# Kernel tuning notes

Measured on AMD Instinct MI355X. Metric: run time of the kernel, lower is better.

The kernel has to match this reference:

```python
import jax, jax.numpy as jnp
import numpy as np

POI, EMB, UNITS, QDIM, B = 5000, 256, 512, 256, 64


def setup_inputs() -> dict:
    key = jax.random.key(0)
    ks = jax.random.split(key, 16)
    s = 0.05
    return {
        "x": jax.random.randint(ks[0], (B,), 0, POI),
        "query": jax.random.normal(ks[1], (B, QDIM), jnp.float32),
        "poi_embedding": jax.random.normal(ks[2], (POI, EMB), jnp.float32),
        "A_hat": jax.random.normal(ks[3], (B, B), jnp.float32),
        "dec_hidden": jax.random.normal(ks[4], (B, UNITS), jnp.float32),
        "cat_dec_hidden": jax.random.normal(ks[5], (1, B, UNITS), jnp.float32),
        # GRUCell params (keras order z, r, h; reset_after=True -> bias [2, 3*units])
        "gru_kernel": jax.random.normal(ks[6], (EMB + QDIM, 3 * UNITS), jnp.float32) * s,
        "gru_rec_kernel": jax.random.normal(ks[7], (UNITS, 3 * UNITS), jnp.float32) * s,
        "gru_bias": jax.random.normal(ks[8], (2, 3 * UNITS), jnp.float32) * s,
        # Bahdanau attention params
        "W1_w": jax.random.normal(ks[9], (EMB, UNITS), jnp.float32) * s,
        "W1_b": jnp.zeros((UNITS,), jnp.float32),
        "W2_w": jax.random.normal(ks[10], (UNITS, UNITS), jnp.float32) * s,
        "W2_b": jnp.zeros((UNITS,), jnp.float32),
        "V_w": jax.random.normal(ks[11], (UNITS, 1), jnp.float32) * s,
        "V_b": jnp.zeros((1,), jnp.float32),
        # output dense: concat(context EMB, output_ UNITS, cat_hidden UNITS) -> POI
        "fc_w": jax.random.normal(ks[12], (EMB + 2 * UNITS, POI), jnp.float32) * s,
        "fc_b": jnp.zeros((POI,), jnp.float32),
    }


def _gru_cell(x, h, kernel, rec_kernel, bias):
    # keras GRUCell, reset_after=True, gate order (z, r, h)
    xm = x @ kernel + bias[0]        # [B, 3U]
    hm = h @ rec_kernel + bias[1]    # [B, 3U]
    xz, xr, xh = jnp.split(xm, 3, axis=-1)
    hz, hr, hh = jnp.split(hm, 3, axis=-1)
    z = jax.nn.sigmoid(xz + hz)
    r = jax.nn.sigmoid(xr + hr)
    h_cand = jnp.tanh(xh + r * hh)
    h_new = z * h + (1.0 - z) * h_cand
    return h_new, h_new


def reference(x, query, poi_embedding, A_hat, dec_hidden, cat_dec_hidden,
              gru_kernel, gru_rec_kernel, gru_bias,
              W1_w, W1_b, W2_w, W2_b, V_w, V_b, fc_w, fc_b):
    emb = poi_embedding
    x1 = jnp.concatenate([emb[x], query], axis=1)          # [B, EMB+QDIM]
    output_, state = _gru_cell(x1, dec_hidden, gru_kernel, gru_rec_kernel, gru_bias)
    # Bahdanau attention: values are the full embedding table [POI, EMB]
    v_proj = emb @ W1_w + W1_b                              # [POI, U]
    q_proj = output_ @ W2_w + W2_b                          # [B, U]
    score = jnp.tanh(v_proj[None, :, :] + q_proj[:, None, :]) @ V_w + V_b  # [B, POI, 1]
    attn = jax.nn.softmax(score, axis=1)                    # [B, POI, 1]
    context = jnp.sum(attn * emb[None, :, :], axis=1)       # [B, EMB]
    out_cat = jnp.concatenate([context, output_, cat_dec_hidden[0]], axis=1)
    logits = out_cat @ fc_w + fc_b                          # [B, POI]
    return (logits, state, output_)
```

## Files before the change

### kernel.cpp

```cpp
#include <hip/hip_runtime.h>
#include <hip/hip_bf16.h>

typedef __bf16 bf16;
typedef __bf16 bf16x8 __attribute__((ext_vector_type(8)));
typedef float f32x4 __attribute__((ext_vector_type(4)));

#define BB 64
#define EMB 256
#define UNITS 512
#define POI 5000
#define KCAT 1280
#define SCLD 5024
#define L2E 1.4426950408889634f

__device__ __forceinline__ float rcp_(float x){ return __builtin_amdgcn_rcpf(x); }
__device__ __forceinline__ float exp2_(float x){ return __builtin_amdgcn_exp2f(x); }

__device__ __forceinline__ f32x4 mm16f(const float* __restrict__ A, const float* __restrict__ B,
                                       int lda, int ldb, int K, int mr, int nc, int lane){
  int q = lane >> 4;
  f32x4 acc = {0.f,0.f,0.f,0.f};
  const float* ap = A + (size_t)mr*lda + q*8;
  const float* bp = B + (size_t)(q*8)*ldb + nc;
#pragma unroll 2
  for(int k0 = 0; k0 < K; k0 += 32){
    f32x4 a0 = *(const f32x4*)ap;
    f32x4 a1 = *(const f32x4*)(ap+4);
    bf16x8 a, b;
#pragma unroll
    for(int j=0;j<4;j++){ a[j] = (bf16)a0[j]; a[4+j] = (bf16)a1[j]; }
#pragma unroll
    for(int j=0;j<8;j++) b[j] = (bf16)bp[(size_t)j*ldb];
    acc = __builtin_amdgcn_mfma_f32_16x16x32_bf16(a, b, acc, 0, 0, 0);
    ap += 32; bp += (size_t)32*ldb;
  }
  return acc;
}

__global__ void k_prep(const int* __restrict__ x, const float* __restrict__ query,
                       const float* __restrict__ emb, const float* __restrict__ catd,
                       float* __restrict__ x1, float* __restrict__ outc){
  int b = blockIdx.x, t = threadIdx.x;
  int row = x[b];
  x1[b*512 + t]       = emb[(size_t)row*EMB + t];
  x1[b*512 + 256 + t] = query[(size_t)b*256 + t];
  outc[b*KCAT + 768 + t]       = catd[(size_t)b*512 + t];
  outc[b*KCAT + 768 + 256 + t] = catd[(size_t)b*512 + 256 + t];
}

__global__ __launch_bounds__(256) void k_gru(const float* __restrict__ x1, const float* __restrict__ h0,
    const float* __restrict__ gruK, const float* __restrict__ gruR,
    float* __restrict__ xmP, float* __restrict__ hmP){
  int lane = threadIdx.x & 63, w = threadIdx.x >> 6;
  int col = blockIdx.x*16 + (lane & 15);
  const float* A = blockIdx.y ? h0 : x1;
  const float* B = blockIdx.y ? gruR : gruK;
  float* C = (blockIdx.y ? hmP : xmP) + (size_t)blockIdx.z*BB*1536;
  int z = blockIdx.z;
  f32x4 acc = mm16f(A + z*256, B + (size_t)(z*256)*1536, 512, 1536, 256,
                    w*16 + (lane & 15), col, lane);
  int rb = w*16 + (lane >> 4)*4;
#pragma unroll
  for(int r=0;r<4;r++) C[(size_t)(rb+r)*1536 + col] = acc[r];
}

__global__ void k_gates(const float* __restrict__ xmP, const float* __restrict__ hmP,
                        const float* __restrict__ bias, const float* __restrict__ h0,
                        float* __restrict__ hn, float* __restrict__ outc, float* __restrict__ dout){
  int b = blockIdx.x, u = threadIdx.x;
  const float* x0 = xmP + b*1536; const float* x1s = xmP + (size_t)BB*1536 + b*1536;
  const float* h0s = hmP + b*1536; const float* h1s = hmP + (size_t)BB*1536 + b*1536;
  float xz = x0[u]      + x1s[u]      + bias[u];
  float xg = x0[512+u]  + x1s[512+u]  + bias[512+u];
  float xh = x0[1024+u] + x1s[1024+u] + bias[1024+u];
  float hz = h0s[u]      + h1s[u]      + bias[1536+u];
  float hg = h0s[512+u]  + h1s[512+u]  + bias[2048+u];
  float hh = h0s[1024+u] + h1s[1024+u] + bias[2560+u];
  float z = rcp_(1.f + exp2_(-L2E*(xz+hz)));
  float r = rcp_(1.f + exp2_(-L2E*(xg+hg)));
  float ca = xh + r*hh;
  ca = fminf(fmaxf(ca, -15.f), 15.f);
  float e = exp2_(2.f*L2E*ca);
  float hc = (e - 1.f)*rcp_(e + 1.f);
  float h = h0[b*512+u];
  float v = z*h + (1.f - z)*hc;
  hn[b*512+u] = v;
  outc[b*KCAT + 256 + u] = v;
  dout[(size_t)POI*BB + (size_t)b*512 + u] = v;
  dout[(size_t)POI*BB + (size_t)BB*512 + (size_t)b*512 + u] = v;
}

__global__ __launch_bounds__(256) void k_qproj(const float* __restrict__ hn, const float* __restrict__ W2,
                        const float* __restrict__ W2b, float* __restrict__ Eq){
  int lane = threadIdx.x & 63, w = threadIdx.x >> 6;
  int col = blockIdx.x*16 + (lane & 15);
  f32x4 acc = mm16f(hn, W2, UNITS, UNITS, UNITS, w*16 + (lane & 15), col, lane);
  float bn = W2b[col];
  int rb = w*16 + (lane >> 4)*4;
#pragma unroll
  for(int r=0;r<4;r++){
    float v = (acc[r] + bn)*(2.f*L2E);
    Eq[(rb+r)*UNITS + col] = exp2_(fminf(fmaxf(v, -40.f), 40.f));
  }
}

__global__ __launch_bounds__(256) void k_vscore(const float* __restrict__ emb, const float* __restrict__ W1,
    const float* __restrict__ W1b, const float* __restrict__ Eq,
    const float* __restrict__ Vw, float* __restrict__ scS){
  __shared__ float evs[16][132];
  __shared__ float Qs[64][68];
  __shared__ float vws[128];
  int t = threadIdx.x, lane = t & 63, w = t >> 6;
  int p0 = blockIdx.x*16, uh = blockIdx.y*128;
  int mr = p0 + (lane & 15); if(mr > POI-1) mr = POI-1;
#pragma unroll
  for(int i=0;i<2;i++){
    int ncl = (w + i*4)*16 + (lane & 15);
    f32x4 acc = mm16f(emb, W1, EMB, UNITS, EMB, mr, uh + ncl, lane);
    float bn = W1b[uh + ncl];
    int rb = (lane >> 4)*4;
#pragma unroll
    for(int r=0;r<4;r++){
      float v = (acc[r] + bn)*(2.f*L2E);
      evs[rb+r][ncl] = exp2_(fminf(fmaxf(v, -40.f), 40.f));
    }
  }
  if(t < 128) vws[t] = Vw[uh + t];
  int tp = t & 7, tb = t >> 3;
  float s00=0.f, s01=0.f, s10=0.f, s11=0.f;
  for(int c=0;c<2;c++){
    __syncthreads();
    int ub = c*64;
    for(int i=t;i<4096;i+=256){ int b=i>>6, u=i&63; Qs[b][u] = Eq[b*UNITS + uh + ub + u]; }
    __syncthreads();
#pragma unroll
    for(int u4=0;u4<16;u4++){
      f32x4 e0 = *(f32x4*)&evs[2*tp][ub+u4*4];
      f32x4 e1 = *(f32x4*)&evs[2*tp+1][ub+u4*4];
      f32x4 q0 = *(f32x4*)&Qs[2*tb][u4*4];
      f32x4 q1 = *(f32x4*)&Qs[2*tb+1][u4*4];
      f32x4 w4 = *(f32x4*)&vws[ub+u4*4];
#pragma unroll
      for(int e=0;e<4;e++){
        float wv = w4[e];
        s00 += wv * rcp_(e0[e]*q0[e] + 1.f);
        s01 += wv * rcp_(e0[e]*q1[e] + 1.f);
        s10 += wv * rcp_(e1[e]*q0[e] + 1.f);
        s11 += wv * rcp_(e1[e]*q1[e] + 1.f);
      }
    }
  }
  float* s = scS + (size_t)blockIdx.y*BB*SCLD;
  int pA = p0 + 2*tp, bA = 2*tb;
  if(pA < POI)  { s[(size_t)bA*SCLD + pA]   = s00; s[(size_t)(bA+1)*SCLD + pA]   = s01; }
  if(pA+1 < POI){ s[(size_t)bA*SCLD + pA+1] = s10; s[(size_t)(bA+1)*SCLD + pA+1] = s11; }
}

__global__ __launch_bounds__(512) void k_softmax(float* __restrict__ sc, const float* __restrict__ Vw,
                                                 float* __restrict__ outc){
  __shared__ float red[512];
  int b = blockIdx.x, t = threadIdx.x;
  if(t < 256) outc[b*KCAT + t] = 0.f;
  red[t] = Vw[t];
  __syncthreads();
  for(int o=256;o>0;o>>=1){ if(t<o) red[t]+=red[t+o]; __syncthreads(); }
  float SW = red[0]; __syncthreads();
  float* sA = sc + (size_t)b*SCLD;
  const float* s1 = sA + (size_t)BB*SCLD;
  const float* s2 = sA + (size_t)2*BB*SCLD;
  const float* s3 = sA + (size_t)3*BB*SCLD;
  float mx = -3.4e38f;
  for(int p=t;p<POI;p+=512){
    float s = SW - 2.f*(sA[p] + s1[p] + s2[p] + s3[p]);
    sA[p] = s;
    mx = fmaxf(mx, s);
  }
  red[t] = mx; __syncthreads();
  for(int o=256;o>0;o>>=1){ if(t<o) red[t]=fmaxf(red[t],red[t+o]); __syncthreads(); }
  float M = red[0]; __syncthreads();
  float sum = 0.f;
  for(int p=t;p<POI;p+=512){
    float wv = exp2_((sA[p] - M)*L2E);
    sA[p] = wv;
    sum += wv;
  }
  red[t] = sum; __syncthreads();
  for(int o=256;o>0;o>>=1){ if(t<o) red[t]+=red[t+o]; __syncthreads(); }
  float iv = rcp_(red[0]);
  for(int p=t;p<POI;p+=512) sA[p] *= iv;
  if(t < SCLD-POI) sA[POI + t] = 0.f;
}

__global__ __launch_bounds__(256) void k_ctx(const float* __restrict__ wb, const float* __restrict__ emb,
                                             float* __restrict__ outc){
  int lane = threadIdx.x & 63, w = threadIdx.x >> 6;
  int n = blockIdx.x*16 + (lane & 15);
  int ky = blockIdx.y;
  int kbeg = ky*384;
  int mr = w*16 + (lane & 15);
  f32x4 acc = mm16f(wb + kbeg, emb + (size_t)kbeg*EMB, SCLD, EMB, 384, mr, n, lane);
  if(ky == 12){
    int q = lane >> 4;
    const float* ap = wb + (size_t)mr*SCLD + 4992 + q*8;
    bf16x8 a, bfr;
#pragma unroll
    for(int j=0;j<8;j++) a[j] = (bf16)ap[j];
#pragma unroll
    for(int j=0;j<8;j++){
      int k = 4992 + q*8 + j; int kc = k < POI ? k : POI-1;
      bfr[j] = (bf16)emb[(size_t)kc*EMB + n];
    }
    acc = __builtin_amdgcn_mfma_f32_16x16x32_bf16(a, bfr, acc, 0, 0, 0);
  }
  int rb = w*16 + (lane >> 4)*4;
#pragma unroll
  for(int r=0;r<4;r++) atomicAdd(&outc[(size_t)(rb+r)*KCAT + n], acc[r]);
}

__global__ __launch_bounds__(256) void k_logits(const float* __restrict__ A, const float* __restrict__ Bw,
                        const float* __restrict__ fcb, float* __restrict__ out){
  int lane = threadIdx.x & 63, w = threadIdx.x >> 6;
  int n = blockIdx.x*16 + (lane & 15);
  int nc = n < POI ? n : POI-1;
  int ky = blockIdx.y, kbeg = ky*320;
  f32x4 acc = mm16f(A + kbeg, Bw + (size_t)kbeg*POI, KCAT, POI, 320,
                    w*16 + (lane & 15), nc, lane);
  int rb = w*16 + (lane >> 4)*4;
  if(n < POI){
    float bn = (ky == 0) ? fcb[n] : 0.f;
#pragma unroll
    for(int r=0;r<4;r++) atomicAdd(&out[(size_t)(rb+r)*POI + n], acc[r] + bn);
  }
}

extern "C" void kernel_launch(void* const* d_in, const int* in_sizes, int n_in,
                              void* d_out, int out_size, void* d_ws, size_t ws_size,
                              hipStream_t stream){
  const int*   x     = (const int*)d_in[0];
  const float* query = (const float*)d_in[1];
  const float* emb   = (const float*)d_in[2];
  const float* h0    = (const float*)d_in[4];
  const float* catd  = (const float*)d_in[5];
  const float* gruK  = (const float*)d_in[6];
  const float* gruR  = (const float*)d_in[7];
  const float* gruB  = (const float*)d_in[8];
  const float* W1    = (const float*)d_in[9];
  const float* W1b   = (const float*)d_in[10];
  const float* W2    = (const float*)d_in[11];
  const float* W2b   = (const float*)d_in[12];
  const float* Vw    = (const float*)d_in[13];
  const float* fcw   = (const float*)d_in[15];
  const float* fcb   = (const float*)d_in[16];
  float* out = (float*)d_out;

  char* ws = (char*)d_ws;
  size_t off = 0;
  auto alloc = [&](size_t bytes)->void*{ void* p = ws + off; off += (bytes + 255) & ~(size_t)255; return p; };
  float* x1   = (float*)alloc((size_t)BB*512*4);
  float* outc = (float*)alloc((size_t)BB*KCAT*4);
  float* xmP  = (float*)alloc((size_t)2*BB*1536*4);
  float* hmP  = (float*)alloc((size_t)2*BB*1536*4);
  float* hn   = (float*)alloc((size_t)BB*512*4);
  float* Eq   = (float*)alloc((size_t)BB*512*4);
  float* sc   = (float*)alloc((size_t)4*BB*SCLD*4);

  hipMemsetAsync(out, 0, (size_t)BB*POI*sizeof(float), stream);
  k_prep   <<<BB, 256, 0, stream>>>(x, query, emb, catd, x1, outc);
  k_gru    <<<dim3(96,2,2), 256, 0, stream>>>(x1, h0, gruK, gruR, xmP, hmP);
  k_gates  <<<BB, 512, 0, stream>>>(xmP, hmP, gruB, h0, hn, outc, out);
  k_qproj  <<<32, 256, 0, stream>>>(hn, W2, W2b, Eq);
  k_vscore <<<dim3(313,4), 256, 0, stream>>>(emb, W1, W1b, Eq, Vw, sc);
  k_softmax<<<BB, 512, 0, stream>>>(sc, Vw, outc);
  k_ctx    <<<dim3(16,13), 256, 0, stream>>>(sc, emb, outc);
  k_logits <<<dim3(313,4), 256, 0, stream>>>(outc, fcw, fcb, out);
}
```

Before: 198.5 us.

## Fuse embedding gather into GRU and use atomics with paired reciprocals for attention scores

Removes the k_prep kernel: the GRU GEMM now reads embedding rows and query directly, and the cat_dec_hidden copy moves into the gates kernel. The attention score kernel splits units into 8 chunks of 64 instead of 4 of 128. It accumulates partial scores into one zeroed buffer with atomicAdd instead of four partial buffers. It merges pairs of reciprocals into a single rcp of a product to halve the transcendental count. Softmax drops the constant offset and the max subtraction, relying on scores being bounded by the V weights, and runs with 1024 threads. In exchange it adds atomic traffic, an extra memset and a tighter exp clamp to avoid overflow in the paired products.

```diff
diff --git a/kernel.cpp b/kernel.cpp
--- a/kernel.cpp
+++ b/kernel.cpp
@@ -37,28 +37,25 @@
   return acc;
 }
 
-__global__ void k_prep(const int* __restrict__ x, const float* __restrict__ query,
-                       const float* __restrict__ emb, const float* __restrict__ catd,
-                       float* __restrict__ x1, float* __restrict__ outc){
-  int b = blockIdx.x, t = threadIdx.x;
-  int row = x[b];
-  x1[b*512 + t]       = emb[(size_t)row*EMB + t];
-  x1[b*512 + 256 + t] = query[(size_t)b*256 + t];
-  outc[b*KCAT + 768 + t]       = catd[(size_t)b*512 + t];
-  outc[b*KCAT + 768 + 256 + t] = catd[(size_t)b*512 + 256 + t];
-}
-
-__global__ __launch_bounds__(256) void k_gru(const float* __restrict__ x1, const float* __restrict__ h0,
+__global__ __launch_bounds__(256) void k_gru(const int* __restrict__ x,
+    const float* __restrict__ query, const float* __restrict__ emb, const float* __restrict__ h0,
     const float* __restrict__ gruK, const float* __restrict__ gruR,
     float* __restrict__ xmP, float* __restrict__ hmP){
   int lane = threadIdx.x & 63, w = threadIdx.x >> 6;
   int col = blockIdx.x*16 + (lane & 15);
-  const float* A = blockIdx.y ? h0 : x1;
-  const float* B = blockIdx.y ? gruR : gruK;
-  float* C = (blockIdx.y ? hmP : xmP) + (size_t)blockIdx.z*BB*1536;
+  int m = w*16 + (lane & 15);
   int z = blockIdx.z;
-  f32x4 acc = mm16f(A + z*256, B + (size_t)(z*256)*1536, 512, 1536, 256,
-                    w*16 + (lane & 15), col, lane);
+  const float* A; const float* B; int lda, mr;
+  if(blockIdx.y == 0){
+    B = gruK + (size_t)(z*256)*1536;
+    if(z == 0){ A = emb;   mr = x[m]; lda = EMB; }
+    else      { A = query; mr = m;    lda = 256; }
+  } else {
+    B = gruR + (size_t)(z*256)*1536;
+    A = h0 + z*256; mr = m; lda = UNITS;
+  }
+  f32x4 acc = mm16f(A, B, lda, 1536, 256, mr, col, lane);
+  float* C = (blockIdx.y ? hmP : xmP) + (size_t)z*BB*1536;
   int rb = w*16 + (lane >> 4)*4;
 #pragma unroll
   for(int r=0;r<4;r++) C[(size_t)(rb+r)*1536 + col] = acc[r];
@@ -66,6 +63,7 @@
 
 __global__ void k_gates(const float* __restrict__ xmP, const float* __restrict__ hmP,
                         const float* __restrict__ bias, const float* __restrict__ h0,
+                        const float* __restrict__ catd,
                         float* __restrict__ hn, float* __restrict__ outc, float* __restrict__ dout){
   int b = blockIdx.x, u = threadIdx.x;
   const float* x0 = xmP + b*1536; const float* x1s = xmP + (size_t)BB*1536 + b*1536;
@@ -86,6 +84,7 @@
   float v = z*h + (1.f - z)*hc;
   hn[b*512+u] = v;
   outc[b*KCAT + 256 + u] = v;
+  outc[b*KCAT + 768 + u] = catd[(size_t)b*512 + u];
   dout[(size_t)POI*BB + (size_t)b*512 + u] = v;
   dout[(size_t)POI*BB + (size_t)BB*512 + (size_t)b*512 + u] = v;
 }
@@ -100,94 +99,83 @@
 #pragma unroll
   for(int r=0;r<4;r++){
     float v = (acc[r] + bn)*(2.f*L2E);
-    Eq[(rb+r)*UNITS + col] = exp2_(fminf(fmaxf(v, -40.f), 40.f));
+    Eq[(rb+r)*UNITS + col] = exp2_(fminf(fmaxf(v, -28.f), 28.f));
   }
 }
 
 __global__ __launch_bounds__(256) void k_vscore(const float* __restrict__ emb, const float* __restrict__ W1,
     const float* __restrict__ W1b, const float* __restrict__ Eq,
-    const float* __restrict__ Vw, float* __restrict__ scS){
-  __shared__ float evs[16][132];
+    const float* __restrict__ Vw, float* __restrict__ sc){
+  __shared__ float evs[16][68];
   __shared__ float Qs[64][68];
-  __shared__ float vws[128];
+  __shared__ float vws[64];
   int t = threadIdx.x, lane = t & 63, w = t >> 6;
-  int p0 = blockIdx.x*16, uh = blockIdx.y*128;
+  int p0 = blockIdx.x*16, uh = blockIdx.y*64;
   int mr = p0 + (lane & 15); if(mr > POI-1) mr = POI-1;
-#pragma unroll
-  for(int i=0;i<2;i++){
-    int ncl = (w + i*4)*16 + (lane & 15);
+  {
+    int ncl = w*16 + (lane & 15);
     f32x4 acc = mm16f(emb, W1, EMB, UNITS, EMB, mr, uh + ncl, lane);
     float bn = W1b[uh + ncl];
     int rb = (lane >> 4)*4;
 #pragma unroll
     for(int r=0;r<4;r++){
       float v = (acc[r] + bn)*(2.f*L2E);
-      evs[rb+r][ncl] = exp2_(fminf(fmaxf(v, -40.f), 40.f));
+      evs[rb+r][ncl] = exp2_(fminf(fmaxf(v, -28.f), 28.f));
     }
   }
-  if(t < 128) vws[t] = Vw[uh + t];
+  for(int i=t;i<1024;i+=256){ int b=i>>4, u4=i&15; *(f32x4*)&Qs[b][u4*4] = *(const f32x4*)&Eq[b*UNITS + uh + u4*4]; }
+  if(t < 64) vws[t] = Vw[uh + t];
+  __syncthreads();
   int tp = t & 7, tb = t >> 3;
   float s00=0.f, s01=0.f, s10=0.f, s11=0.f;
-  for(int c=0;c<2;c++){
-    __syncthreads();
-    int ub = c*64;
-    for(int i=t;i<4096;i+=256){ int b=i>>6, u=i&63; Qs[b][u] = Eq[b*UNITS + uh + ub + u]; }
-    __syncthreads();
-#pragma unroll
-    for(int u4=0;u4<16;u4++){
-      f32x4 e0 = *(f32x4*)&evs[2*tp][ub+u4*4];
-      f32x4 e1 = *(f32x4*)&evs[2*tp+1][ub+u4*4];
-      f32x4 q0 = *(f32x4*)&Qs[2*tb][u4*4];
-      f32x4 q1 = *(f32x4*)&Qs[2*tb+1][u4*4];
-      f32x4 w4 = *(f32x4*)&vws[ub+u4*4];
-#pragma unroll
-      for(int e=0;e<4;e++){
-        float wv = w4[e];
-        s00 += wv * rcp_(e0[e]*q0[e] + 1.f);
-        s01 += wv * rcp_(e0[e]*q1[e] + 1.f);
-        s10 += wv * rcp_(e1[e]*q0[e] + 1.f);
-        s11 += wv * rcp_(e1[e]*q1[e] + 1.f);
-      }
+#pragma unroll
+  for(int u4=0;u4<16;u4++){
+    f32x4 e0 = *(f32x4*)&evs[2*tp][u4*4];
+    f32x4 e1 = *(f32x4*)&evs[2*tp+1][u4*4];
+    f32x4 q0 = *(f32x4*)&Qs[2*tb][u4*4];
+    f32x4 q1 = *(f32x4*)&Qs[2*tb+1][u4*4];
+    f32x4 w4 = *(f32x4*)&vws[u4*4];
+#pragma unroll
+    for(int h=0;h<2;h++){
+      int i0 = 2*h, i1 = 2*h+1;
+      float w0 = w4[i0], w1 = w4[i1];
+      float da, db;
+      da = __builtin_fmaf(e0[i0], q0[i0], 1.f); db = __builtin_fmaf(e0[i1], q0[i1], 1.f);
+      s00 = __builtin_fmaf(__builtin_fmaf(w0, db, w1*da), rcp_(da*db), s00);
+      da = __builtin_fmaf(e0[i0], q1[i0], 1.f); db = __builtin_fmaf(e0[i1], q1[i1], 1.f);
+      s01 = __builtin_fmaf(__builtin_fmaf(w0, db, w1*da), rcp_(da*db), s01);
+      da = __builtin_fmaf(e1[i0], q0[i0], 1.f); db = __builtin_fmaf(e1[i1], q0[i1], 1.f);
+      s10 = __builtin_fmaf(__builtin_fmaf(w0, db, w1*da), rcp_(da*db), s10);
+      da = __builtin_fmaf(e1[i0], q1[i0], 1.f); db = __builtin_fmaf(e1[i1], q1[i1], 1.f);
+      s11 = __builtin_fmaf(__builtin_fmaf(w0, db, w1*da), rcp_(da*db), s11);
     }
   }
-  float* s = scS + (size_t)blockIdx.y*BB*SCLD;
   int pA = p0 + 2*tp, bA = 2*tb;
-  if(pA < POI)  { s[(size_t)bA*SCLD + pA]   = s00; s[(size_t)(bA+1)*SCLD + pA]   = s01; }
-  if(pA+1 < POI){ s[(size_t)bA*SCLD + pA+1] = s10; s[(size_t)(bA+1)*SCLD + pA+1] = s11; }
-}
-
-__global__ __launch_bounds__(512) void k_softmax(float* __restrict__ sc, const float* __restrict__ Vw,
-                                                 float* __restrict__ outc){
-  __shared__ float red[512];
+  if(pA < POI){
+    atomicAdd(&sc[(size_t)bA*SCLD + pA],     s00);
+    atomicAdd(&sc[(size_t)(bA+1)*SCLD + pA], s01);
+  }
+  if(pA+1 < POI){
+    atomicAdd(&sc[(size_t)bA*SCLD + pA+1],     s10);
+    atomicAdd(&sc[(size_t)(bA+1)*SCLD + pA+1], s11);
+  }
+}
+
+__global__ __launch_bounds__(1024) void k_softmax(float* __restrict__ sc, float* __restrict__ outc){
+  __shared__ float red[1024];
   int b = blockIdx.x, t = threadIdx.x;
   if(t < 256) outc[b*KCAT + t] = 0.f;
-  red[t] = Vw[t];
-  __syncthreads();
-  for(int o=256;o>0;o>>=1){ if(t<o) red[t]+=red[t+o]; __syncthreads(); }
-  float SW = red[0]; __syncthreads();
   float* sA = sc + (size_t)b*SCLD;
-  const float* s1 = sA + (size_t)BB*SCLD;
-  const float* s2 = sA + (size_t)2*BB*SCLD;
-  const float* s3 = sA + (size_t)3*BB*SCLD;
-  float mx = -3.4e38f;
-  for(int p=t;p<POI;p+=512){
-    float s = SW - 2.f*(sA[p] + s1[p] + s2[p] + s3[p]);
-    sA[p] = s;
-    mx = fmaxf(mx, s);
-  }
-  red[t] = mx; __syncthreads();
-  for(int o=256;o>0;o>>=1){ if(t<o) red[t]=fmaxf(red[t],red[t+o]); __syncthreads(); }
-  float M = red[0]; __syncthreads();
   float sum = 0.f;
-  for(int p=t;p<POI;p+=512){
-    float wv = exp2_((sA[p] - M)*L2E);
+  for(int p=t;p<POI;p+=1024){
+    float wv = exp2_(-2.f*L2E*sA[p]);
     sA[p] = wv;
     sum += wv;
   }
   red[t] = sum; __syncthreads();
-  for(int o=256;o>0;o>>=1){ if(t<o) red[t]+=red[t+o]; __syncthreads(); }
+  for(int o=512;o>0;o>>=1){ if(t<o) red[t]+=red[t+o]; __syncthreads(); }
   float iv = rcp_(red[0]);
-  for(int p=t;p<POI;p+=512) sA[p] *= iv;
+  for(int p=t;p<POI;p+=1024) sA[p] *= iv;
   if(t < SCLD-POI) sA[POI + t] = 0.f;
 }
 
@@ -256,21 +244,20 @@
   char* ws = (char*)d_ws;
   size_t off = 0;
   auto alloc = [&](size_t bytes)->void*{ void* p = ws + off; off += (bytes + 255) & ~(size_t)255; return p; };
-  float* x1   = (float*)alloc((size_t)BB*512*4);
   float* outc = (float*)alloc((size_t)BB*KCAT*4);
   float* xmP  = (float*)alloc((size_t)2*BB*1536*4);
   float* hmP  = (float*)alloc((size_t)2*BB*1536*4);
   float* hn   = (float*)alloc((size_t)BB*512*4);
   float* Eq   = (float*)alloc((size_t)BB*512*4);
-  float* sc   = (float*)alloc((size_t)4*BB*SCLD*4);
-
-  hipMemsetAsync(out, 0, (size_t)BB*POI*sizeof(float), stream);
-  k_prep   <<<BB, 256, 0, stream>>>(x, query, emb, catd, x1, outc);
-  k_gru    <<<dim3(96,2,2), 256, 0, stream>>>(x1, h0, gruK, gruR, xmP, hmP);
-  k_gates  <<<BB, 512, 0, stream>>>(xmP, hmP, gruB, h0, hn, outc, out);
+  float* sc   = (float*)alloc((size_t)BB*SCLD*4);
+
+  hipMemsetAsync(out, 0, (size_t)BB*POI*4, stream);
+  hipMemsetAsync(sc, 0, (size_t)BB*SCLD*4, stream);
+  k_gru    <<<dim3(96,2,2), 256, 0, stream>>>(x, query, emb, h0, gruK, gruR, xmP, hmP);
+  k_gates  <<<BB, 512, 0, stream>>>(xmP, hmP, gruB, h0, catd, hn, outc, out);
   k_qproj  <<<32, 256, 0, stream>>>(hn, W2, W2b, Eq);
-  k_vscore <<<dim3(313,4), 256, 0, stream>>>(emb, W1, W1b, Eq, Vw, sc);
-  k_softmax<<<BB, 512, 0, stream>>>(sc, Vw, outc);
+  k_vscore <<<dim3(313,8), 256, 0, stream>>>(emb, W1, W1b, Eq, Vw, sc);
+  k_softmax<<<BB, 1024, 0, stream>>>(sc, outc);
   k_ctx    <<<dim3(16,13), 256, 0, stream>>>(sc, emb, outc);
   k_logits <<<dim3(313,4), 256, 0, stream>>>(outc, fcw, fcb, out);
 }
```

Result: slower. 229.2 us (+15.5%).
